# Kernel tuning notes

Hardware: AMD Instinct MI355X
Metric: run time of the kernel (lower is better)

Reference implementation:

```python
import math
import jax, jax.numpy as jnp
import numpy as np

DIM = 96
HEADS = 3
HEAD_DIM = DIM // HEADS
WS = 8            # window_size
SHIFT = 4         # shift_size
N = WS * WS       # tokens per window
SCALE = HEAD_DIM ** (-0.5)


def _relative_positions_log():
    # matches WindowAttention.get_relative_positions (torch.meshgrid ij)
    coords = jnp.stack(jnp.meshgrid(jnp.arange(WS), jnp.arange(WS), indexing='ij'))  # [2,WS,WS]
    flat = coords.reshape(2, -1)                                # [2,N]
    rel = flat[:, :, None] - flat[:, None, :]                   # [2,N,N]
    rel = jnp.transpose(rel, (1, 2, 0)).astype(jnp.float32)     # [N,N,2]
    return jnp.sign(rel) * jnp.log1p(jnp.abs(rel))


def _conv1x1(x, w, b):
    # x: [B,C,H,W], w: [O,C], b: [O]
    return jnp.einsum('bchw,oc->bohw', x, w) + b[:, None, None]


def _conv3x3_reflect(x, w, b):
    # reflect padding=1, kernel 3x3
    xp = jnp.pad(x, ((0, 0), (0, 0), (1, 1), (1, 1)), mode='reflect')
    y = jax.lax.conv_general_dilated(xp, w, (1, 1), 'VALID',
                                     dimension_numbers=('NCHW', 'OIHW', 'NCHW'))
    return y + b[None, :, None, None]


def setup_inputs() -> dict:
    key = jax.random.key(0)
    ks = jax.random.split(key, 16)
    s = 0.02
    inp = {
        'x':      jax.random.normal(ks[0], (8, DIM, 256, 256), jnp.float32),
        'V_w':    jax.random.normal(ks[1], (DIM, DIM), jnp.float32) * s,
        'V_b':    jnp.zeros((DIM,), jnp.float32),
        'QK_w':   jax.random.normal(ks[2], (2 * DIM, DIM), jnp.float32) * s,
        'QK_b':   jnp.zeros((2 * DIM,), jnp.float32),
        'conv_w': jax.random.normal(ks[3], (DIM, DIM, 3, 3), jnp.float32) * s,
        'conv_b': jnp.zeros((DIM,), jnp.float32),
        'proj_w': jax.random.normal(ks[4], (DIM, DIM), jnp.float32) * s,
        'proj_b': jnp.zeros((DIM,), jnp.float32),
        'm1_w':   jax.random.normal(ks[5], (256, 2), jnp.float32) * 0.1,
        'm1_b':   jnp.zeros((256,), jnp.float32),
        'm2_w':   jax.random.normal(ks[6], (HEADS, 256), jnp.float32) * 0.1,
        'm2_b':   jnp.zeros((HEADS,), jnp.float32),
    }
    return inp


def reference(x, V_w, V_b, QK_w, QK_b, conv_w, conv_b, proj_w, proj_b,
              m1_w, m1_b, m2_w, m2_b):
    B, C, H, W = x.shape
    V = _conv1x1(x, V_w, V_b)                     # [B,C,H,W]
    QK = _conv1x1(x, QK_w, QK_b)                  # [B,2C,H,W]
    QKV = jnp.concatenate([QK, V], axis=1)        # [B,3C,H,W]

    # check_size with shift: H,W divisible by WS -> mod_pad = 0
    pad_r = (WS - SHIFT) % WS
    QKV = jnp.pad(QKV, ((0, 0), (0, 0), (SHIFT, pad_r), (SHIFT, pad_r)), mode='reflect')
    Ht, Wt = QKV.shape[2], QKV.shape[3]

    # window partition -> [B*nH*nW, N, 3C]
    sQ = jnp.transpose(QKV, (0, 2, 3, 1))         # [B,Ht,Wt,3C]
    nH, nW = Ht // WS, Wt // WS
    qkv = sQ.reshape(B, nH, WS, nW, WS, 3 * C)
    qkv = jnp.transpose(qkv, (0, 1, 3, 2, 4, 5)).reshape(-1, N, 3 * C)

    # window attention with MLP relative-position bias
    Bw = qkv.shape[0]
    qkv = qkv.reshape(Bw, N, 3, HEADS, HEAD_DIM)
    qkv = jnp.transpose(qkv, (2, 0, 3, 1, 4))     # [3,Bw,h,N,d]
    q, k, v = qkv[0], qkv[1], qkv[2]

    rel = _relative_positions_log()               # [N,N,2]
    hbias = jax.nn.gelu(rel @ m1_w.T + m1_b, approximate=False)
    bias = hbias @ m2_w.T + m2_b                  # [N,N,h]
    bias = jnp.transpose(bias, (2, 0, 1))         # [h,N,N]

    attn = jnp.einsum('bhnd,bhmd->bhnm', q, k) * SCALE + bias[None]
    attn = jax.nn.softmax(attn, axis=-1)
    xw = jnp.einsum('bhnm,bhmd->bhnd', attn, v)   # [Bw,h,N,d]
    xw = jnp.transpose(xw, (0, 2, 1, 3)).reshape(Bw, N, C)

    # window reverse -> [B,Ht,Wt,C]
    xr = xw.reshape(B, nH, nW, WS, WS, C)
    xr = jnp.transpose(xr, (0, 1, 3, 2, 4, 5)).reshape(B, Ht, Wt, C)
    attn_out = xr[:, SHIFT:SHIFT + H, SHIFT:SHIFT + W, :]
    attn_out = jnp.transpose(attn_out, (0, 3, 1, 2))   # [B,C,H,W]

    conv_out = _conv3x3_reflect(V, conv_w, conv_b)
    x_out = _conv1x1(conv_out + attn_out, proj_w, proj_b)
    return x_out
```

## Files before the change

kernel.cpp:

```cpp
#include <hip/hip_runtime.h>
#include <cstdint>

using u16 = unsigned short;
using u32 = unsigned int;
using f32x4  = __attribute__((ext_vector_type(4))) float;
using bf16x8 = __attribute__((ext_vector_type(8))) short;

#define NHEADS 3
#define WSZ 8
#define IMG 256
#define NPX 65536
#define NWIN 33
#define ATT_SCALE 0.17677669529663687f
#define INV_SCALE 5.656854249492381f
#define HALO_PITCH 104

__device__ __forceinline__ int refl(int i, int n) {
    return i < 0 ? -i : (i >= n ? 2*n - 2 - i : i);
}
__device__ __forceinline__ float bflo(u32 u){ union{u32 i; float f;} x; x.i = u << 16; return x.f; }
__device__ __forceinline__ float bfhi(u32 u){ union{u32 i; float f;} x; x.i = u & 0xffff0000u; return x.f; }
__device__ __forceinline__ float bf2f(u16 v){ union{u32 i; float f;} x; x.i = ((u32)v) << 16; return x.f; }
__device__ __forceinline__ u16 f2bf(float f){
    union{float f; u32 i;} x; x.f = f;
    u32 r = x.i + 0x7fffu + ((x.i >> 16) & 1u);
    return (u16)(r >> 16);
}
__device__ __forceinline__ u32 pk2bf(float a, float b){
    return (u32)f2bf(a) | ((u32)f2bf(b) << 16);
}

__global__ __launch_bounds__(256) void k_bias(
    const float* __restrict__ m1w, const float* __restrict__ m1b,
    const float* __restrict__ m2w, const float* __restrict__ m2b,
    float* __restrict__ biasS)
{
    int idx = blockIdx.x * 256 + threadIdx.x;
    int hh  = idx >> 12;
    int rem = idx & 4095;
    int n = rem >> 6, m = rem & 63;
    int di = (n >> 3) - (m >> 3);
    int dj = (n & 7)  - (m & 7);
    float fdi = copysignf(log1pf(fabsf((float)di)), (float)di);
    float fdj = copysignf(log1pf(fabsf((float)dj)), (float)dj);
    float acc = m2b[hh];
    for (int k = 0; k < 256; ++k) {
        float tv = fdi * m1w[2*k] + fdj * m1w[2*k+1] + m1b[k];
        float g  = 0.5f * tv * (1.0f + erff(tv * 0.70710678118654752f));
        acc = fmaf(g, m2w[hh*256 + k], acc);
    }
    biasS[hh*4096 + n*64 + m] = acc * INV_SCALE;
}

__global__ __launch_bounds__(64) void k_wprep(
    const float* __restrict__ cw, u16* __restrict__ Bfrag)
{
    int ks   = blockIdx.x;
    int lane = threadIdx.x;
    int nt    = ks % 6;
    int kstep = ks / 6;
    int tap   = kstep % 9;
    int ck    = kstep / 9;
    int dy = tap / 3, dx = tap % 3;
    int cout = nt*16 + (lane & 15);
    int cin0 = ck*32 + (lane >> 4)*8;
    u16* dst = Bfrag + (size_t)ks*512 + lane*8;
    #pragma unroll
    for (int j = 0; j < 8; ++j)
        dst[j] = f2bf(cw[((size_t)(cout*96 + cin0 + j))*9 + dy*3 + dx]);
}

__global__ __launch_bounds__(64) void k_wprep_qkv(
    const float* __restrict__ qkw, const float* __restrict__ vw,
    u16* __restrict__ BfragQ)
{
    int ks   = blockIdx.x;
    int lane = threadIdx.x;
    int nt    = ks % 18;
    int kstep = ks / 18;
    int o     = nt*16 + (lane & 15);
    int cin0  = kstep*32 + (lane >> 4)*8;
    const float* src = (o < 192) ? (qkw + (size_t)o*96 + cin0)
                                 : (vw + (size_t)(o - 192)*96 + cin0);
    u16* dst = BfragQ + (size_t)ks*512 + lane*8;
    #pragma unroll
    for (int j = 0; j < 8; ++j) dst[j] = f2bf(src[j]);
}

__global__ __launch_bounds__(64) void k_wprep_proj(
    const float* __restrict__ pw, u16* __restrict__ BfragP)
{
    int ks   = blockIdx.x;
    int lane = threadIdx.x;
    int nt    = ks % 6;
    int kstep = ks / 6;
    int o     = nt*16 + (lane & 15);
    int cin0  = kstep*32 + (lane >> 4)*8;
    u16* dst = BfragP + (size_t)ks*512 + lane*8;
    #pragma unroll
    for (int j = 0; j < 8; ++j) dst[j] = f2bf(pw[(size_t)o*96 + cin0 + j]);
}

__global__ __launch_bounds__(256, 2) void k_qkv(
    const float* __restrict__ x, const u16* __restrict__ BfragQ,
    const float* __restrict__ qkb, const float* __restrict__ vb,
    u16* __restrict__ qkv)
{
    int tile = blockIdx.x;
    int b    = tile >> 8;
    int pix0 = (tile & 255) * 256;
    size_t px0 = (size_t)tile * 256;
    int t    = threadIdx.x;

    __shared__ u16 xs[256 * HALO_PITCH];

    {
        const float* xb = x + (size_t)b*96*NPX + pix0 + t;
        u16* xrow = xs + t * HALO_PITCH;
        float v[96];
        #pragma unroll
        for (int c = 0; c < 96; ++c) v[c] = xb[(size_t)c * NPX];
        #pragma unroll
        for (int oct = 0; oct < 12; ++oct) {
            uint4 o;
            o.x = pk2bf(v[oct*8+0], v[oct*8+1]);
            o.y = pk2bf(v[oct*8+2], v[oct*8+3]);
            o.z = pk2bf(v[oct*8+4], v[oct*8+5]);
            o.w = pk2bf(v[oct*8+6], v[oct*8+7]);
            *(uint4*)(xrow + oct*8) = o;
        }
    }
    __syncthreads();

    int wv   = __builtin_amdgcn_readfirstlane(t >> 6);
    int lane = t & 63;
    int lc   = lane & 15;
    int kg   = lane >> 4;

    const u16* bbase = BfragQ + lane*8;

    #pragma unroll 1
    for (int og = 0; og < 3; ++og) {
        f32x4 acc[4][6] = {};
        #pragma unroll
        for (int kstep = 0; kstep < 3; ++kstep) {
            bf16x8 bF[6];
            #pragma unroll
            for (int nt = 0; nt < 6; ++nt)
                bF[nt] = *(const bf16x8*)(bbase + (size_t)(kstep*18 + og*6 + nt)*512);
            #pragma unroll
            for (int mt = 0; mt < 4; ++mt) {
                bf16x8 aF = *(const bf16x8*)(xs + (wv*64 + mt*16 + lc)*HALO_PITCH + kstep*32 + kg*8);
                #pragma unroll
                for (int nt = 0; nt < 6; ++nt)
                    acc[mt][nt] = __builtin_amdgcn_mfma_f32_16x16x32_bf16(aF, bF[nt], acc[mt][nt], 0, 0, 0);
            }
        }

        float bv[6];
        #pragma unroll
        for (int nt = 0; nt < 6; ++nt) {
            int o = og*96 + nt*16 + lc;
            bv[nt] = (o < 192) ? qkb[o] : vb[o - 192];
        }

        #pragma unroll
        for (int mt = 0; mt < 4; ++mt) {
            #pragma unroll
            for (int r = 0; r < 4; ++r) {
                size_t px = px0 + wv*64 + mt*16 + kg*4 + r;
                u16* qp = qkv + px*288 + og*96 + lc;
                #pragma unroll
                for (int nt = 0; nt < 6; ++nt)
                    qp[nt*16] = f2bf(acc[mt][nt][r] + bv[nt]);
            }
        }
    }
}

__global__ __launch_bounds__(256, 2) void k_attn(
    const u16* __restrict__ qkv, const float* __restrict__ biasS,
    u16* __restrict__ att)
{
    __shared__ u16 lds[27648];
    int t    = threadIdx.x;
    int wv   = __builtin_amdgcn_readfirstlane(t >> 6);
    int lane = t & 63;
    int lc   = lane & 15;
    int kg   = lane >> 4;

    u16* Plds = lds + wv * 6912;
    u16* Vlds = Plds + 4608;

    int win = blockIdx.x * 4 + wv;
    int b   = win / 1089;
    int wr  = win - b * 1089;
    int wy  = wr / NWIN;
    int wx  = wr - wy * NWIN;

    int py = wy*8 + (lane >> 3) - 4;
    int px = wx*8 + (lane & 7)  - 4;
    int iy = refl(py, IMG), ix = refl(px, IMG);
    int pxoff = b*NPX + iy*256 + ix;
    int vpx = (py >= 0 && py < IMG && px >= 0 && px < IMG) ? pxoff : (int)(pxoff | 0x80000000u);

    int pxA[4];
    #pragma unroll
    for (int mt = 0; mt < 4; ++mt)
        pxA[mt] = __builtin_amdgcn_ds_bpermute((16*mt + lc)*4, vpx) & 0x7fffffff;

    #pragma unroll 1
    for (int h = 0; h < 3; ++h) {
        {
            const u16* vrow = qkv + (size_t)pxoff*288 + 192 + h*32;
            #pragma unroll
            for (int g = 0; g < 4; ++g) {
                bf16x8 vv = *(const bf16x8*)(vrow + g*8);
                #pragma unroll
                for (int j = 0; j < 8; ++j)
                    Vlds[(g*8 + j)*72 + lane] = (u16)vv[j];
            }
        }

        bf16x8 afr[4], bfr[4];
        #pragma unroll
        for (int mt = 0; mt < 4; ++mt) {
            afr[mt] = *(const bf16x8*)(qkv + (size_t)pxA[mt]*288 + 96 + h*32 + kg*8);
            bfr[mt] = *(const bf16x8*)(qkv + (size_t)pxA[mt]*288 +      h*32 + kg*8);
        }

        f32x4 acc[4][4];
        const float* bb = biasS + h*4096 + lc*64 + 4*kg;
        #pragma unroll
        for (int nt = 0; nt < 4; ++nt)
            #pragma unroll
            for (int mt = 0; mt < 4; ++mt)
                acc[mt][nt] = *(const f32x4*)(bb + nt*1024 + mt*16);

        #pragma unroll
        for (int mt = 0; mt < 4; ++mt)
            #pragma unroll
            for (int nt = 0; nt < 4; ++nt)
                acc[mt][nt] = __builtin_amdgcn_mfma_f32_16x16x32_bf16(afr[mt], bfr[nt], acc[mt][nt], 0, 0, 0);

        #pragma unroll
        for (int nt = 0; nt < 4; ++nt) {
            float m = acc[0][nt][0];
            #pragma unroll
            for (int mt = 0; mt < 4; ++mt)
                #pragma unroll
                for (int r = 0; r < 4; ++r)
                    m = fmaxf(m, acc[mt][nt][r]);
            m = fmaxf(m, __shfl_xor(m, 16));
            m = fmaxf(m, __shfl_xor(m, 32));
            float s = 0.f;
            #pragma unroll
            for (int mt = 0; mt < 4; ++mt)
                #pragma unroll
                for (int r = 0; r < 4; ++r) {
                    float p = __expf((acc[mt][nt][r] - m) * ATT_SCALE);
                    acc[mt][nt][r] = p;
                    s += p;
                }
            s += __shfl_xor(s, 16);
            s += __shfl_xor(s, 32);
            float inv = 1.0f / s;
            #pragma unroll
            for (int mt = 0; mt < 4; ++mt)
                #pragma unroll
                for (int r = 0; r < 4; ++r)
                    acc[mt][nt][r] *= inv;
        }

        #pragma unroll
        for (int nt = 0; nt < 4; ++nt)
            #pragma unroll
            for (int mt = 0; mt < 4; ++mt) {
                uint2 pk;
                pk.x = pk2bf(acc[mt][nt][0], acc[mt][nt][1]);
                pk.y = pk2bf(acc[mt][nt][2], acc[mt][nt][3]);
                *(uint2*)(Plds + (16*nt + lc)*72 + 16*mt + 4*kg) = pk;
            }

        f32x4 oacc[4][2] = {};
        #pragma unroll
        for (int s = 0; s < 2; ++s) {
            bf16x8 vb2[2];
            #pragma unroll
            for (int ntpv = 0; ntpv < 2; ++ntpv)
                vb2[ntpv] = *(const bf16x8*)(Vlds + (16*ntpv + lc)*72 + s*32 + kg*8);
            #pragma unroll
            for (int mtpv = 0; mtpv < 4; ++mtpv) {
                bf16x8 pa = *(const bf16x8*)(Plds + (16*mtpv + lc)*72 + s*32 + kg*8);
                #pragma unroll
                for (int ntpv = 0; ntpv < 2; ++ntpv)
                    oacc[mtpv][ntpv] = __builtin_amdgcn_mfma_f32_16x16x32_bf16(pa, vb2[ntpv], oacc[mtpv][ntpv], 0, 0, 0);
            }
        }

        #pragma unroll
        for (int mtpv = 0; mtpv < 4; ++mtpv)
            #pragma unroll
            for (int rr = 0; rr < 4; ++rr) {
                int vp = __builtin_amdgcn_ds_bpermute((16*mtpv + 4*kg + rr)*4, vpx);
                if (vp >= 0) {
                    u16* op = att + (size_t)vp*96 + h*32 + lc;
                    op[0]  = f2bf(oacc[mtpv][0][rr]);
                    op[16] = f2bf(oacc[mtpv][1][rr]);
                }
            }
    }
}

__global__ __launch_bounds__(256, 2) void k_convproj(
    const u16* __restrict__ qkv, const u16* __restrict__ att,
    const u16* __restrict__ Bfrag, const float* __restrict__ cb,
    const u16* __restrict__ BfragP, const float* __restrict__ pb,
    float* __restrict__ out)
{
    int tile = blockIdx.x;
    int b    = tile >> 8;
    int tr   = tile & 255;
    int ty0  = (tr >> 3) * 8;
    int tx0  = (tr & 7) * 32;
    int t    = threadIdx.x;

    __shared__ u16 vt[340 * HALO_PITCH];

    for (int p = t; p < 340; p += 256) {
        int hr = p / 34;
        int hc = p - hr * 34;
        int gy = refl(ty0 - 1 + hr, IMG);
        int gx = refl(tx0 - 1 + hc, IMG);
        const uint4* src = (const uint4*)(qkv + ((size_t)(b*NPX + gy*256 + gx))*288 + 192);
        uint4* dst = (uint4*)(vt + p * HALO_PITCH);
        #pragma unroll
        for (int q = 0; q < 12; ++q) dst[q] = src[q];
    }
    __syncthreads();

    int wv   = __builtin_amdgcn_readfirstlane(t >> 6);
    int lane = t & 63;
    int lc   = lane & 15;
    int kg   = lane >> 4;

    int abase[4];
    #pragma unroll
    for (int mt = 0; mt < 4; ++mt) {
        int r_mt = 2*wv + (mt >> 1);
        int c_mt = (mt & 1) * 16;
        abase[mt] = (r_mt*34 + c_mt + lc) * HALO_PITCH + kg*8;
    }

    f32x4 acc[4][6] = {};

    const u16* bfr = Bfrag + lane*8;
    #pragma unroll 1
    for (int ck = 0; ck < 3; ++ck) {
        const u16* bck = bfr + ck * 27648;
        int aoff = ck * 32;
        #pragma unroll
        for (int tap = 0; tap < 9; ++tap) {
            const int dy = tap / 3, dx = tap % 3;
            bf16x8 bF[6];
            #pragma unroll
            for (int nt = 0; nt < 6; ++nt)
                bF[nt] = *(const bf16x8*)(bck + (tap*6 + nt)*512);
            #pragma unroll
            for (int mt = 0; mt < 4; ++mt) {
                bf16x8 aF = *(const bf16x8*)(vt + abase[mt] + aoff + (dy*34 + dx)*HALO_PITCH);
                #pragma unroll
                for (int nt = 0; nt < 6; ++nt)
                    acc[mt][nt] = __builtin_amdgcn_mfma_f32_16x16x32_bf16(aF, bF[nt], acc[mt][nt], 0, 0, 0);
            }
        }
    }

    float cbv[6];
    #pragma unroll
    for (int nt = 0; nt < 6; ++nt) cbv[nt] = cb[nt*16 + lc];

    __syncthreads();

    #pragma unroll
    for (int mt = 0; mt < 4; ++mt) {
        int r_mt = 2*wv + (mt >> 1);
        int c_mt = (mt & 1) * 16;
        int y    = ty0 + r_mt;
        #pragma unroll
        for (int r = 0; r < 4; ++r) {
            int x  = tx0 + c_mt + kg*4 + r;
            int pl = r_mt*32 + c_mt + kg*4 + r;
            size_t pbase = ((size_t)(b*NPX + y*256 + x))*96 + lc;
            u16* srow = vt + pl * HALO_PITCH + lc;
            #pragma unroll
            for (int nt = 0; nt < 6; ++nt) {
                float v = acc[mt][nt][r] + cbv[nt] + bf2f(att[pbase + nt*16]);
                srow[nt*16] = f2bf(v);
            }
        }
    }
    __syncthreads();

    f32x4 pacc[4][6] = {};
    const u16* bbase = BfragP + lane*8;
    #pragma unroll
    for (int kstep = 0; kstep < 3; ++kstep) {
        bf16x8 bF[6];
        #pragma unroll
        for (int nt = 0; nt < 6; ++nt)
            bF[nt] = *(const bf16x8*)(bbase + (size_t)(kstep*6 + nt)*512);
        #pragma unroll
        for (int mt = 0; mt < 4; ++mt) {
            bf16x8 aF = *(const bf16x8*)(vt + (wv*64 + mt*16 + lc)*HALO_PITCH + kstep*32 + kg*8);
            #pragma unroll
            for (int nt = 0; nt < 6; ++nt)
                pacc[mt][nt] = __builtin_amdgcn_mfma_f32_16x16x32_bf16(aF, bF[nt], pacc[mt][nt], 0, 0, 0);
        }
    }

    float bv[6];
    #pragma unroll
    for (int nt = 0; nt < 6; ++nt) bv[nt] = pb[nt*16 + lc];

    float* ob = out + (size_t)b*96*NPX;
    #pragma unroll
    for (int mt = 0; mt < 4; ++mt) {
        #pragma unroll
        for (int r = 0; r < 4; ++r) {
            int pl = wv*64 + mt*16 + kg*4 + r;
            int y  = ty0 + (pl >> 5);
            int x  = tx0 + (pl & 31);
            #pragma unroll
            for (int nt = 0; nt < 6; ++nt)
                ob[(size_t)(nt*16 + lc)*NPX + y*256 + x] = pacc[mt][nt][r] + bv[nt];
        }
    }
}

extern "C" void kernel_launch(void* const* d_in, const int* in_sizes, int n_in,
                              void* d_out, int out_size, void* d_ws, size_t ws_size,
                              hipStream_t stream)
{
    const float* x      = (const float*)d_in[0];
    const float* V_w    = (const float*)d_in[1];
    const float* V_b    = (const float*)d_in[2];
    const float* QK_w   = (const float*)d_in[3];
    const float* QK_b   = (const float*)d_in[4];
    const float* conv_w = (const float*)d_in[5];
    const float* conv_b = (const float*)d_in[6];
    const float* proj_w = (const float*)d_in[7];
    const float* proj_b = (const float*)d_in[8];
    const float* m1_w   = (const float*)d_in[9];
    const float* m1_b   = (const float*)d_in[10];
    const float* m2_w   = (const float*)d_in[11];
    const float* m2_b   = (const float*)d_in[12];
    float* out = (float*)d_out;

    char* ws = (char*)d_ws;
    float* biasS = (float*)ws;
    u16* qkvb = (u16*)(ws + 49152);
    u16* attb = (u16*)(ws + 49152 + 301989888);
    char* scr = ws + 49152 + 301989888 + 100663296;

    u16* Bfrag  = (u16*)scr;
    u16* BfragQ = (u16*)(scr + (1 << 20));
    u16* BfragP = (u16*)(scr + (2 << 20));

    hipLaunchKernelGGL(k_wprep,      dim3(162),     dim3(64),  0, stream, conv_w, Bfrag);
    hipLaunchKernelGGL(k_wprep_qkv,  dim3(54),      dim3(64),  0, stream, QK_w, V_w, BfragQ);
    hipLaunchKernelGGL(k_wprep_proj, dim3(18),      dim3(64),  0, stream, proj_w, BfragP);
    hipLaunchKernelGGL(k_bias,       dim3(48),      dim3(256), 0, stream, m1_w, m1_b, m2_w, m2_b, biasS);
    hipLaunchKernelGGL(k_qkv,        dim3(2048),    dim3(256), 0, stream, x, BfragQ, QK_b, V_b, qkvb);
    hipLaunchKernelGGL(k_attn,       dim3(2178),    dim3(256), 0, stream, qkvb, biasS, attb);
    hipLaunchKernelGGL(k_convproj,   dim3(2048),    dim3(256), 0, stream, qkvb, attb, Bfrag, conv_b, BfragP, proj_b, out);
}
```

Measured before the change: 523.8 us.

## Process attention query tiles one at a time to shrink registers and LDS

The window-attention kernel now loops over the four 16-query tiles serially instead of holding the full 64x64 score matrix in registers. Per tile it does the QK MFMAs, the softmax, stages a 16-row P slice in LDS and runs the PV MFMAs. This shrinks per-wave LDS from 6912 to 3456 elements and cuts accumulator registers, so launch bounds are raised to 4 blocks per CU to increase occupancy. The cost is a serialized, non-unrolled inner loop with less instruction-level parallelism, plus repeated V fragment loads from LDS for each tile.

```diff
diff --git a/kernel.cpp b/kernel.cpp
--- a/kernel.cpp
+++ b/kernel.cpp
@@ -178,19 +178,19 @@
     }
 }
 
-__global__ __launch_bounds__(256, 2) void k_attn(
+__global__ __launch_bounds__(256, 4) void k_attn(
     const u16* __restrict__ qkv, const float* __restrict__ biasS,
     u16* __restrict__ att)
 {
-    __shared__ u16 lds[27648];
+    __shared__ u16 lds[4 * 3456];
     int t    = threadIdx.x;
     int wv   = __builtin_amdgcn_readfirstlane(t >> 6);
     int lane = t & 63;
     int lc   = lane & 15;
     int kg   = lane >> 4;
 
-    u16* Plds = lds + wv * 6912;
-    u16* Vlds = Plds + 4608;
+    u16* Plds = lds + wv * 3456;
+    u16* Vlds = Plds + 1152;
 
     int win = blockIdx.x * 4 + wv;
     int b   = win / 1089;
@@ -222,35 +222,31 @@
             }
         }
 
-        bf16x8 afr[4], bfr[4];
-        #pragma unroll
-        for (int mt = 0; mt < 4; ++mt) {
+        bf16x8 afr[4];
+        #pragma unroll
+        for (int mt = 0; mt < 4; ++mt)
             afr[mt] = *(const bf16x8*)(qkv + (size_t)pxA[mt]*288 + 96 + h*32 + kg*8);
-            bfr[mt] = *(const bf16x8*)(qkv + (size_t)pxA[mt]*288 +      h*32 + kg*8);
-        }
-
-        f32x4 acc[4][4];
-        const float* bb = biasS + h*4096 + lc*64 + 4*kg;
-        #pragma unroll
-        for (int nt = 0; nt < 4; ++nt)
+
+        #pragma unroll 1
+        for (int nt = 0; nt < 4; ++nt) {
+            bf16x8 qf = *(const bf16x8*)(qkv + (size_t)pxA[nt]*288 + h*32 + kg*8);
+
+            f32x4 acc[4];
+            const float* bb = biasS + h*4096 + (size_t)nt*1024 + lc*64 + 4*kg;
             #pragma unroll
             for (int mt = 0; mt < 4; ++mt)
-                acc[mt][nt] = *(const f32x4*)(bb + nt*1024 + mt*16);
-
-        #pragma unroll
-        for (int mt = 0; mt < 4; ++mt)
-            #pragma unroll
-            for (int nt = 0; nt < 4; ++nt)
-                acc[mt][nt] = __builtin_amdgcn_mfma_f32_16x16x32_bf16(afr[mt], bfr[nt], acc[mt][nt], 0, 0, 0);
-
-        #pragma unroll
-        for (int nt = 0; nt < 4; ++nt) {
-            float m = acc[0][nt][0];
+                acc[mt] = *(const f32x4*)(bb + mt*16);
+
             #pragma unroll
             for (int mt = 0; mt < 4; ++mt)
+                acc[mt] = __builtin_amdgcn_mfma_f32_16x16x32_bf16(afr[mt], qf, acc[mt], 0, 0, 0);
+
+            float m = acc[0][0];
+            #pragma unroll
+            for (int mt = 0; mt < 4; ++mt)
                 #pragma unroll
                 for (int r = 0; r < 4; ++r)
-                    m = fmaxf(m, acc[mt][nt][r]);
+                    m = fmaxf(m, acc[mt][r]);
             m = fmaxf(m, __shfl_xor(m, 16));
             m = fmaxf(m, __shfl_xor(m, 32));
             float s = 0.f;
@@ -258,8 +254,8 @@
             for (int mt = 0; mt < 4; ++mt)
                 #pragma unroll
                 for (int r = 0; r < 4; ++r) {
-                    float p = __expf((acc[mt][nt][r] - m) * ATT_SCALE);
-                    acc[mt][nt][r] = p;
+                    float p = __expf((acc[mt][r] - m) * ATT_SCALE);
+                    acc[mt][r] = p;
                     s += p;
                 }
             s += __shfl_xor(s, 16);
@@ -269,46 +265,37 @@
             for (int mt = 0; mt < 4; ++mt)
                 #pragma unroll
                 for (int r = 0; r < 4; ++r)
-                    acc[mt][nt][r] *= inv;
-        }
-
-        #pragma unroll
-        for (int nt = 0; nt < 4; ++nt)
+                    acc[mt][r] *= inv;
+
             #pragma unroll
             for (int mt = 0; mt < 4; ++mt) {
                 uint2 pk;
-                pk.x = pk2bf(acc[mt][nt][0], acc[mt][nt][1]);
-                pk.y = pk2bf(acc[mt][nt][2], acc[mt][nt][3]);
-                *(uint2*)(Plds + (16*nt + lc)*72 + 16*mt + 4*kg) = pk;
-            }
-
-        f32x4 oacc[4][2] = {};
-        #pragma unroll
-        for (int s = 0; s < 2; ++s) {
-            bf16x8 vb2[2];
-            #pragma unroll
-            for (int ntpv = 0; ntpv < 2; ++ntpv)
-                vb2[ntpv] = *(const bf16x8*)(Vlds + (16*ntpv + lc)*72 + s*32 + kg*8);
-            #pragma unroll
-            for (int mtpv = 0; mtpv < 4; ++mtpv) {
-                bf16x8 pa = *(const bf16x8*)(Plds + (16*mtpv + lc)*72 + s*32 + kg*8);
-                #pragma unroll
-                for (int ntpv = 0; ntpv < 2; ++ntpv)
-                    oacc[mtpv][ntpv] = __builtin_amdgcn_mfma_f32_16x16x32_bf16(pa, vb2[ntpv], oacc[mtpv][ntpv], 0, 0, 0);
-            }
-        }
-
-        #pragma unroll
-        for (int mtpv = 0; mtpv < 4; ++mtpv)
+                pk.x = pk2bf(acc[mt][0], acc[mt][1]);
+                pk.y = pk2bf(acc[mt][2], acc[mt][3]);
+                *(uint2*)(Plds + lc*72 + 16*mt + 4*kg) = pk;
+            }
+
+            f32x4 oacc[2] = {};
+            #pragma unroll
+            for (int s2 = 0; s2 < 2; ++s2) {
+                bf16x8 pa = *(const bf16x8*)(Plds + lc*72 + s2*32 + kg*8);
+                #pragma unroll
+                for (int ntpv = 0; ntpv < 2; ++ntpv) {
+                    bf16x8 vb2 = *(const bf16x8*)(Vlds + (16*ntpv + lc)*72 + s2*32 + kg*8);
+                    oacc[ntpv] = __builtin_amdgcn_mfma_f32_16x16x32_bf16(pa, vb2, oacc[ntpv], 0, 0, 0);
+                }
+            }
+
             #pragma unroll
             for (int rr = 0; rr < 4; ++rr) {
-                int vp = __builtin_amdgcn_ds_bpermute((16*mtpv + 4*kg + rr)*4, vpx);
+                int vp = __builtin_amdgcn_ds_bpermute((16*nt + 4*kg + rr)*4, vpx);
                 if (vp >= 0) {
                     u16* op = att + (size_t)vp*96 + h*32 + lc;
-                    op[0]  = f2bf(oacc[mtpv][0][rr]);
-                    op[16] = f2bf(oacc[mtpv][1][rr]);
+                    op[0]  = f2bf(oacc[0][rr]);
+                    op[16] = f2bf(oacc[1][rr]);
                 }
             }
+        }
     }
 }
 
```

Measured after the change: 516.4 us. No clear change (-1.4%).
